# Performance work log

Hardware: AMD Instinct MI355X
Metric: run time of the kernel (lower is better)

## Reference

```python
import jax, jax.numpy as jnp
import numpy as np

TEMP = 10.0  # self.temp in the module


def _l2norm(x, eps):
    # matches torch cosine_similarity / F.normalize eps-clamped L2 normalization
    n = jnp.sqrt(jnp.sum(x * x, axis=-1, keepdims=True))
    return x / jnp.maximum(n, eps)


def setup_inputs() -> dict:
    key = jax.random.key(0)
    k1, k2, k3, k4 = jax.random.split(key, 4)
    b, n, k, q, t, c = 2, 5, 5, 75, 196, 384  # 5-way 5-shot, 15 queries/way, ViT-S tokens
    return {
        "feat_shot": jax.random.normal(k1, (b, n, k, t, c), jnp.float32),
        "feat_query": jax.random.normal(k2, (b, q, t, c), jnp.float32),
        "x_shot": jax.random.normal(k3, (b, n, k, c), jnp.float32),
        "x_query": jax.random.normal(k4, (b, q, c), jnp.float32),
    }


def reference(feat_shot, feat_query, x_shot, x_query):
    b, n, k, t, c = feat_shot.shape
    # --- token-level cosine similarity branch ---
    fq = _l2norm(feat_query, 1e-8)                      # [b,q,t,c]
    fs = _l2norm(feat_shot.reshape(b, n, k * t, c), 1e-8)  # [b,n,k*t,c]
    # cosine sim of every query token vs every shot token of each class
    sim = jnp.einsum('bqtc,bnsc->bqnts', fq, fs)        # [b,q,n,t,k*t]
    # topk(k=1) over shot tokens -> max; .mean(-1) over the size-1 topk dim is identity;
    # then mean over query tokens t
    logits = jnp.max(sim, axis=-1).mean(axis=-1)        # [b,q,n]
    # --- global-feature classifier branch ---
    proto = _l2norm(x_shot.mean(axis=-2), 1e-12)        # prototype mean over k shots: [b,n,c]
    xq = _l2norm(x_query, 1e-12)                        # [b,q,c]
    cls_logits = TEMP * jnp.einsum('bqc,bnc->bqn', xq, proto)  # [b,q,n]
    return (logits, cls_logits)
```

## Files before the change

kernel.cpp:

```cpp
#include <hip/hip_runtime.h>
#include <hip/hip_bf16.h>
#include <hip/hip_fp8.h>
#include <stdint.h>


typedef __attribute__((ext_vector_type(8))) int int8v;
typedef __attribute__((ext_vector_type(4))) float f32x4;

__device__ __forceinline__ unsigned enc_f(float f) {
    unsigned b = __float_as_uint(f);
    return (b & 0x80000000u) ? ~b : (b | 0x80000000u);
}
__device__ __forceinline__ float dec_f(unsigned u) {
    unsigned b = (u & 0x80000000u) ? (u & 0x7FFFFFFFu) : ~u;
    return __uint_as_float(b);
}

__device__ __forceinline__ unsigned pack4_fp8(float a, float b, float c, float d) {
    int r = __builtin_amdgcn_cvt_pk_fp8_f32(a, b, 0, false);
    r = __builtin_amdgcn_cvt_pk_fp8_f32(c, d, r, true);
    return (unsigned)r;
}

__global__ void prep_kernel(const float* __restrict__ feat_query,
                            const float* __restrict__ feat_shot,
                            const float* __restrict__ x_shot,
                            unsigned* __restrict__ fqn,
                            unsigned* __restrict__ fsnp,
                            float* __restrict__ proto,
                            unsigned* __restrict__ P) {
    const int blk  = blockIdx.x;
    const int tid  = threadIdx.x;
    const int lane = tid & 63;
    const int wv   = tid >> 6;

    if (blk < 2478) {
        const int tr  = blk * 16 + wv * 4 + (lane >> 4);
        const int l16 = lane & 15;
        if (tr >= 39640) return;

        const float* row;
        unsigned* o32;
        bool zero = false;
        bool shot = false;
        if (tr < 29400) {
            row = feat_query + (size_t)tr * 384;
            o32 = fqn + (size_t)tr * 96;
        } else {
            const int sp = tr - 29400;
            const int bn = sp >> 10;
            const int s  = sp & 1023;
            row  = feat_shot + ((size_t)bn * 980 + s) * 384;
            zero = (s >= 980);
            shot = true;
            const int shh   = s >> 9;
            const int c     = s & 511;
            const int chunk = c >> 5;
            const int cl    = c & 31;
            o32 = fsnp + (size_t)bn * 98304 + shh * 49152 + chunk * 3072
                       + (cl >> 4) * 512 + (cl & 15) * 4;
        }
        int idxs[6];
#pragma unroll
        for (int j = 0; j < 6; ++j)
            idxs[j] = shot ? ((j >> 1) * 1024 + ((l16 >> 2) & 1) * 256
                              + (((j & 1) << 1) + (l16 >> 3)) * 64 + (l16 & 3))
                           : (l16 + 16 * j);

        if (zero) {
#pragma unroll
            for (int j = 0; j < 6; ++j) o32[idxs[j]] = 0u;
            return;
        }
        const float4* rf4 = (const float4*)row;
        float4 v[6];
        float ss = 0.f;
#pragma unroll
        for (int j = 0; j < 6; ++j) {
            v[j] = rf4[l16 + 16 * j];
            ss += v[j].x * v[j].x + v[j].y * v[j].y + v[j].z * v[j].z + v[j].w * v[j].w;
        }
#pragma unroll
        for (int off = 1; off < 16; off <<= 1) ss += __shfl_xor(ss, off, 64);
        const float sc = 1.0f / fmaxf(sqrtf(ss), 1e-8f);
#pragma unroll
        for (int j = 0; j < 6; ++j)
            o32[idxs[j]] = pack4_fp8(v[j].x * sc, v[j].y * sc, v[j].z * sc, v[j].w * sc);
    } else if (blk < 2481) {
        const int gw = (blk - 2478) * 4 + wv;
        if (gw >= 10) return;
        const float* base = x_shot + (size_t)gw * 5 * 384;
        float v[6];
        float ss = 0.f;
#pragma unroll
        for (int j = 0; j < 6; ++j) {
            float s = 0.f;
#pragma unroll
            for (int kk = 0; kk < 5; ++kk) s += base[kk * 384 + lane + 64 * j];
            s *= 0.2f;
            v[j] = s;
            ss += s * s;
        }
#pragma unroll
        for (int off = 1; off < 64; off <<= 1) ss += __shfl_xor(ss, off, 64);
        const float scale = 1.0f / fmaxf(sqrtf(ss), 1e-12f);
#pragma unroll
        for (int j = 0; j < 6; ++j) proto[(size_t)gw * 384 + lane + 64 * j] = v[j] * scale;
    } else {
        const int i = (blk - 2481) * 256 + tid;
        if (i < 147000) P[i] = 0u;
    }
}

__global__ __launch_bounds__(256, 2) void gemm_kernel(const uint8_t* __restrict__ fqn,
                                                      const uint8_t* __restrict__ fsnp,
                                                      unsigned* __restrict__ P) {
    const int bid = blockIdx.x;
    const int mt  = bid % 58;
    const int g1  = bid / 58;
    const int sh  = g1 & 1;
    const int bc  = g1 >> 1;
    const int b   = bc / 5;
    const int m0  = mt * 256;

    const int tid  = threadIdx.x;
    const int lane = tid & 63;
    const int wv   = tid >> 6;
    const int l15  = lane & 15;
    const int hi   = lane >> 4;

    const uint8_t* Ag = fqn  + (size_t)b * 14700 * 384;
    const uint8_t* Bg = fsnp + (size_t)bc * 393216 + (size_t)sh * 196608;
    const uint8_t* bp = Bg + lane * 16;

    int8v A[4][3];
#pragma unroll
    for (int mi = 0; mi < 4; ++mi) {
        int row = m0 + wv * 64 + mi * 16 + l15;
        row = row < 14700 ? row : 14699;
        const uint8_t* pa = Ag + (size_t)row * 384 + hi * 32;
#pragma unroll
        for (int ks = 0; ks < 3; ++ks) {
            const uint4 x = *(const uint4*)(pa + ks * 128);
            const uint4 y = *(const uint4*)(pa + ks * 128 + 16);
            A[mi][ks] = (int8v){(int)x.x, (int)x.y, (int)x.z, (int)x.w,
                                (int)y.x, (int)y.y, (int)y.z, (int)y.w};
        }
    }

    float rmax[4][4];
#pragma unroll
    for (int mi = 0; mi < 4; ++mi)
#pragma unroll
        for (int i = 0; i < 4; ++i) rmax[mi][i] = -3.0e38f;

    uint4 nx0 = *(const uint4*)(bp);
    uint4 ny0 = *(const uint4*)(bp + 1024);
    uint4 nx1 = *(const uint4*)(bp + 2048);
    uint4 ny1 = *(const uint4*)(bp + 3072);

    for (int chunk = 0; chunk < 16; ++chunk) {
        f32x4 acc[4][2];
#pragma unroll
        for (int mi = 0; mi < 4; ++mi)
#pragma unroll
            for (int nf = 0; nf < 2; ++nf) acc[mi][nf] = (f32x4){0.f, 0.f, 0.f, 0.f};

#pragma unroll
        for (int ks = 0; ks < 3; ++ks) {
            const int8v Bf0 = (int8v){(int)nx0.x, (int)nx0.y, (int)nx0.z, (int)nx0.w,
                                      (int)ny0.x, (int)ny0.y, (int)ny0.z, (int)ny0.w};
            const int8v Bf1 = (int8v){(int)nx1.x, (int)nx1.y, (int)nx1.z, (int)nx1.w,
                                      (int)ny1.x, (int)ny1.y, (int)ny1.z, (int)ny1.w};
            const int kk  = chunk * 3 + ks;
            const int kkn = (kk + 1 < 48) ? kk + 1 : 47;
            const uint8_t* p = bp + (size_t)kkn * 4096;
            nx0 = *(const uint4*)(p);
            ny0 = *(const uint4*)(p + 1024);
            nx1 = *(const uint4*)(p + 2048);
            ny1 = *(const uint4*)(p + 3072);
#pragma unroll
            for (int mi = 0; mi < 4; ++mi) {
                acc[mi][0] = __builtin_amdgcn_mfma_scale_f32_16x16x128_f8f6f4(
                    A[mi][ks], Bf0, acc[mi][0],
                    0, 0, 0, 0x7F7F7F7F, 0, 0x7F7F7F7F);
                acc[mi][1] = __builtin_amdgcn_mfma_scale_f32_16x16x128_f8f6f4(
                    A[mi][ks], Bf1, acc[mi][1],
                    0, 0, 0, 0x7F7F7F7F, 0, 0x7F7F7F7F);
            }
        }

#pragma unroll
        for (int nf = 0; nf < 2; ++nf) {
            if (sh * 512 + chunk * 32 + nf * 16 + l15 < 980) {
#pragma unroll
                for (int mi = 0; mi < 4; ++mi)
#pragma unroll
                    for (int i = 0; i < 4; ++i)
                        rmax[mi][i] = fmaxf(rmax[mi][i], acc[mi][nf][i]);
            }
        }
    }

#pragma unroll
    for (int mi = 0; mi < 4; ++mi)
#pragma unroll
        for (int i = 0; i < 4; ++i) {
            float v = rmax[mi][i];
#pragma unroll
            for (int off = 1; off < 16; off <<= 1) v = fmaxf(v, __shfl_xor(v, off, 64));
            if (l15 == 0) {
                const int row = m0 + wv * 64 + mi * 16 + hi * 4 + i;
                if (row < 14700)
                    atomicMax(&P[(size_t)bc * 14700 + row], enc_f(v));
            }
        }
}

__global__ void final_kernel(const unsigned* __restrict__ P,
                             const float* __restrict__ xq,
                             const float* __restrict__ proto,
                             float* __restrict__ out) {
    const int blk  = blockIdx.x;
    const int tid  = threadIdx.x;
    const int lane = tid & 63;
    const int wv   = tid >> 6;

    if (blk < 188) {
        const int gw = blk * 4 + wv;
        if (gw >= 750) return;
        const int n  = gw % 5;
        const int bq = gw / 5;
        const int b  = bq / 75;
        const int q  = bq % 75;
        const unsigned* row = P + (size_t)(b * 5 + n) * 14700 + q * 196;
        float s = 0.f;
        for (int t = lane; t < 196; t += 64) s += dec_f(row[t]);
#pragma unroll
        for (int off = 1; off < 64; off <<= 1) s += __shfl_xor(s, off, 64);
        if (lane == 0) out[gw] = s * (1.0f / 196.0f);
    } else {
        const int gw = (blk - 188) * 4 + wv;
        if (gw >= 150) return;
        const float* row = xq + (size_t)gw * 384;
        float u[6];
        float ss = 0.f;
#pragma unroll
        for (int j = 0; j < 6; ++j) { u[j] = row[lane + 64 * j]; ss += u[j] * u[j]; }
#pragma unroll
        for (int off = 1; off < 64; off <<= 1) ss += __shfl_xor(ss, off, 64);
        const float scale = 1.0f / fmaxf(sqrtf(ss), 1e-12f);
#pragma unroll
        for (int j = 0; j < 6; ++j) u[j] *= scale;
        const int b = gw / 75;
        for (int n = 0; n < 5; ++n) {
            const float* p = proto + (size_t)(b * 5 + n) * 384;
            float d = 0.f;
#pragma unroll
            for (int j = 0; j < 6; ++j) d += u[j] * p[lane + 64 * j];
#pragma unroll
            for (int off = 1; off < 64; off <<= 1) d += __shfl_xor(d, off, 64);
            if (lane == 0) out[750 + gw * 5 + n] = 10.0f * d;
        }
    }
}

extern "C" void kernel_launch(void* const* d_in, const int* in_sizes, int n_in,
                              void* d_out, int out_size, void* d_ws, size_t ws_size,
                              hipStream_t stream) {
    const float* feat_shot  = (const float*)d_in[0];
    const float* feat_query = (const float*)d_in[1];
    const float* x_shot     = (const float*)d_in[2];
    const float* x_query    = (const float*)d_in[3];
    float* out = (float*)d_out;
    char* ws = (char*)d_ws;

    uint8_t*  fqn   = (uint8_t*)ws;
    uint8_t*  fsnp  = (uint8_t*)(ws + 11289600);
    float*    proto = (float*)(ws + 15221760);
    unsigned* P     = (unsigned*)(ws + 15237120);

    prep_kernel<<<3056, 256, 0, stream>>>(feat_query, feat_shot, x_shot,
                                          (unsigned*)fqn, (unsigned*)fsnp, proto, P);
    gemm_kernel<<<1160, 256, 0, stream>>>(fqn, fsnp, P);
    final_kernel<<<226, 256, 0, stream>>>(P, x_query, proto, out);
}
```

Before: 167.9 us.

## Switch FP8 GEMM to 32x32x64 scaled MFMA with matching shot layout

Replaces the 16x16x128 scaled FP8 MFMA tiles with 32x32x64 MFMA tiles, rewriting the shot-feature packing in the prep kernel to match the new B-fragment layout. B fragments for a whole 32-column chunk are prefetched into registers. The second half of each class's shot tokens runs only 15 chunks instead of 16, skipping an all-padding chunk. The row-max reduction now spans 32 lanes with a different row mapping. The intent is fewer MFMA issues and less wasted work, at the cost of more accumulator and prefetch registers.

```diff
diff --git a/kernel.cpp b/kernel.cpp
--- a/kernel.cpp
+++ b/kernel.cpp
@@ -5,7 +5,7 @@
 
 
 typedef __attribute__((ext_vector_type(8))) int int8v;
-typedef __attribute__((ext_vector_type(4))) float f32x4;
+typedef __attribute__((ext_vector_type(16))) float f32x16;
 
 __device__ __forceinline__ unsigned enc_f(float f) {
     unsigned b = __float_as_uint(f);
@@ -54,17 +54,15 @@
             zero = (s >= 980);
             shot = true;
             const int shh   = s >> 9;
-            const int c     = s & 511;
-            const int chunk = c >> 5;
-            const int cl    = c & 31;
+            const int c9    = s & 511;
+            const int chunk = c9 >> 5;
             o32 = fsnp + (size_t)bn * 98304 + shh * 49152 + chunk * 3072
-                       + (cl >> 4) * 512 + (cl & 15) * 4;
+                       + ((l16 >> 3) * 32 + (c9 & 31)) * 4 + (l16 & 3);
         }
         int idxs[6];
 #pragma unroll
         for (int j = 0; j < 6; ++j)
-            idxs[j] = shot ? ((j >> 1) * 1024 + ((l16 >> 2) & 1) * 256
-                              + (((j & 1) << 1) + (l16 >> 3)) * 64 + (l16 & 3))
+            idxs[j] = shot ? ((2 * j + ((l16 >> 2) & 1)) * 256)
                            : (l16 + 16 * j);
 
         if (zero) {
@@ -126,91 +124,89 @@
     const int tid  = threadIdx.x;
     const int lane = tid & 63;
     const int wv   = tid >> 6;
-    const int l15  = lane & 15;
-    const int hi   = lane >> 4;
+    const int l31  = lane & 31;
+    const int kh   = lane >> 5;
 
     const uint8_t* Ag = fqn  + (size_t)b * 14700 * 384;
     const uint8_t* Bg = fsnp + (size_t)bc * 393216 + (size_t)sh * 196608;
     const uint8_t* bp = Bg + lane * 16;
 
-    int8v A[4][3];
-#pragma unroll
-    for (int mi = 0; mi < 4; ++mi) {
-        int row = m0 + wv * 64 + mi * 16 + l15;
+    int8v A[2][6];
+#pragma unroll
+    for (int mi = 0; mi < 2; ++mi) {
+        int row = m0 + wv * 64 + mi * 32 + l31;
         row = row < 14700 ? row : 14699;
-        const uint8_t* pa = Ag + (size_t)row * 384 + hi * 32;
-#pragma unroll
-        for (int ks = 0; ks < 3; ++ks) {
-            const uint4 x = *(const uint4*)(pa + ks * 128);
-            const uint4 y = *(const uint4*)(pa + ks * 128 + 16);
+        const uint8_t* pa = Ag + (size_t)row * 384 + kh * 32;
+#pragma unroll
+        for (int ks = 0; ks < 6; ++ks) {
+            const uint4 x = *(const uint4*)(pa + ks * 64);
+            const uint4 y = *(const uint4*)(pa + ks * 64 + 16);
             A[mi][ks] = (int8v){(int)x.x, (int)x.y, (int)x.z, (int)x.w,
                                 (int)y.x, (int)y.y, (int)y.z, (int)y.w};
         }
     }
 
-    float rmax[4][4];
-#pragma unroll
-    for (int mi = 0; mi < 4; ++mi)
-#pragma unroll
-        for (int i = 0; i < 4; ++i) rmax[mi][i] = -3.0e38f;
-
-    uint4 nx0 = *(const uint4*)(bp);
-    uint4 ny0 = *(const uint4*)(bp + 1024);
-    uint4 nx1 = *(const uint4*)(bp + 2048);
-    uint4 ny1 = *(const uint4*)(bp + 3072);
-
-    for (int chunk = 0; chunk < 16; ++chunk) {
-        f32x4 acc[4][2];
-#pragma unroll
-        for (int mi = 0; mi < 4; ++mi)
-#pragma unroll
-            for (int nf = 0; nf < 2; ++nf) acc[mi][nf] = (f32x4){0.f, 0.f, 0.f, 0.f};
-
-#pragma unroll
-        for (int ks = 0; ks < 3; ++ks) {
-            const int8v Bf0 = (int8v){(int)nx0.x, (int)nx0.y, (int)nx0.z, (int)nx0.w,
-                                      (int)ny0.x, (int)ny0.y, (int)ny0.z, (int)ny0.w};
-            const int8v Bf1 = (int8v){(int)nx1.x, (int)nx1.y, (int)nx1.z, (int)nx1.w,
-                                      (int)ny1.x, (int)ny1.y, (int)ny1.z, (int)ny1.w};
-            const int kk  = chunk * 3 + ks;
-            const int kkn = (kk + 1 < 48) ? kk + 1 : 47;
-            const uint8_t* p = bp + (size_t)kkn * 4096;
-            nx0 = *(const uint4*)(p);
-            ny0 = *(const uint4*)(p + 1024);
-            nx1 = *(const uint4*)(p + 2048);
-            ny1 = *(const uint4*)(p + 3072);
-#pragma unroll
-            for (int mi = 0; mi < 4; ++mi) {
-                acc[mi][0] = __builtin_amdgcn_mfma_scale_f32_16x16x128_f8f6f4(
-                    A[mi][ks], Bf0, acc[mi][0],
-                    0, 0, 0, 0x7F7F7F7F, 0, 0x7F7F7F7F);
-                acc[mi][1] = __builtin_amdgcn_mfma_scale_f32_16x16x128_f8f6f4(
-                    A[mi][ks], Bf1, acc[mi][1],
-                    0, 0, 0, 0x7F7F7F7F, 0, 0x7F7F7F7F);
+    float rmax[2][16];
+#pragma unroll
+    for (int mi = 0; mi < 2; ++mi)
+#pragma unroll
+        for (int i = 0; i < 16; ++i) rmax[mi][i] = -3.0e38f;
+
+    uint4 SL[6], SH[6];
+#pragma unroll
+    for (int ks = 0; ks < 6; ++ks) {
+        const uint8_t* p = bp + ks * 2048;
+        SL[ks] = *(const uint4*)(p);
+        SH[ks] = *(const uint4*)(p + 1024);
+    }
+
+    const int nchunk = (sh == 1) ? 15 : 16;
+
+    for (int chunk = 0; chunk < nchunk; ++chunk) {
+        f32x16 acc0 = (f32x16)(0.f), acc1 = (f32x16)(0.f);
+        const size_t nb = (size_t)((chunk + 1 < nchunk) ? chunk + 1 : chunk) * 12288;
+
+#pragma unroll
+        for (int ks = 0; ks < 6; ++ks) {
+            const int8v Bf = (int8v){(int)SL[ks].x, (int)SL[ks].y,
+                                     (int)SL[ks].z, (int)SL[ks].w,
+                                     (int)SH[ks].x, (int)SH[ks].y,
+                                     (int)SH[ks].z, (int)SH[ks].w};
+            acc0 = __builtin_amdgcn_mfma_scale_f32_32x32x64_f8f6f4(
+                A[0][ks], Bf, acc0, 0, 0, 0, 0x7F7F7F7F, 0, 0x7F7F7F7F);
+            acc1 = __builtin_amdgcn_mfma_scale_f32_32x32x64_f8f6f4(
+                A[1][ks], Bf, acc1, 0, 0, 0, 0x7F7F7F7F, 0, 0x7F7F7F7F);
+            const uint8_t* p = bp + nb + ks * 2048;
+            SL[ks] = *(const uint4*)(p);
+            SH[ks] = *(const uint4*)(p + 1024);
+        }
+
+        if (sh == 0 || chunk < 14) {
+#pragma unroll
+            for (int i = 0; i < 16; ++i) {
+                rmax[0][i] = fmaxf(rmax[0][i], acc0[i]);
+                rmax[1][i] = fmaxf(rmax[1][i], acc1[i]);
             }
-        }
-
-#pragma unroll
-        for (int nf = 0; nf < 2; ++nf) {
-            if (sh * 512 + chunk * 32 + nf * 16 + l15 < 980) {
-#pragma unroll
-                for (int mi = 0; mi < 4; ++mi)
-#pragma unroll
-                    for (int i = 0; i < 4; ++i)
-                        rmax[mi][i] = fmaxf(rmax[mi][i], acc[mi][nf][i]);
+        } else if (chunk == 14) {
+            if (l31 < 20) {
+#pragma unroll
+                for (int i = 0; i < 16; ++i) {
+                    rmax[0][i] = fmaxf(rmax[0][i], acc0[i]);
+                    rmax[1][i] = fmaxf(rmax[1][i], acc1[i]);
+                }
             }
         }
     }
 
 #pragma unroll
-    for (int mi = 0; mi < 4; ++mi)
-#pragma unroll
-        for (int i = 0; i < 4; ++i) {
+    for (int mi = 0; mi < 2; ++mi)
+#pragma unroll
+        for (int i = 0; i < 16; ++i) {
             float v = rmax[mi][i];
 #pragma unroll
-            for (int off = 1; off < 16; off <<= 1) v = fmaxf(v, __shfl_xor(v, off, 64));
-            if (l15 == 0) {
-                const int row = m0 + wv * 64 + mi * 16 + hi * 4 + i;
+            for (int off = 1; off < 32; off <<= 1) v = fmaxf(v, __shfl_xor(v, off, 64));
+            if (l31 == 0) {
+                const int row = m0 + wv * 64 + mi * 32 + (i & 3) + 8 * (i >> 2) + 4 * kh;
                 if (row < 14700)
                     atomicMax(&P[(size_t)bc * 14700 + row], enc_f(v));
             }
```

After: 164.4 us. -2.1%, faster.
